# Kernel optimization log

Measured on AMD Instinct MI355X. Metric: run time of the kernel, lower is better.

## Reference

```python
import jax, jax.numpy as jnp
import numpy as np

N, E, DIN, DH, DOUT = 100000, 1600000, 512, 128, 40


def setup_inputs() -> dict:
    key = jax.random.key(0)
    ks = jax.random.split(key, 4)
    x = jax.random.normal(ks[0], (N, DIN), dtype=jnp.float32)
    edge_index = jax.random.randint(ks[1], (2, E), 0, N, dtype=jnp.int32)
    W1 = jax.random.normal(ks[2], (DIN, DH), dtype=jnp.float32) / np.sqrt(DIN).astype(np.float32)
    b1 = jnp.zeros((DH,), jnp.float32)
    W2 = jax.random.normal(ks[3], (DH, DOUT), dtype=jnp.float32) / np.sqrt(DH).astype(np.float32)
    b2 = jnp.zeros((DOUT,), jnp.float32)
    return {"x": x, "edge_index": edge_index, "W1": W1, "b1": b1, "W2": W2, "b2": b2}


def _gcn_conv(x, W, b, src, dst, norm, n):
    # PyG GCNConv: linear transform first, then normalized neighbor aggregation
    h = x @ W                                   # [n, d_out]
    msg = h[src] * norm[:, None]                # gather + scale, [E+n, d_out]
    out = jax.ops.segment_sum(msg, dst, num_segments=n)  # scatter-add
    return out + b


def reference(x, edge_index, W1, b1, W2, b2):
    n = x.shape[0]
    loops = jnp.arange(n, dtype=edge_index.dtype)
    src = jnp.concatenate([edge_index[0], loops])   # with self-loops
    dst = jnp.concatenate([edge_index[1], loops])
    deg = jax.ops.segment_sum(jnp.ones_like(dst, dtype=jnp.float32), dst, num_segments=n)
    dinv = jnp.where(deg > 0, jax.lax.rsqrt(jnp.maximum(deg, 1.0)), 0.0)
    norm = dinv[src] * dinv[dst]                    # deg^{-1/2}[j] * deg^{-1/2}[i]
    h = jax.nn.relu(_gcn_conv(x, W1, b1, src, dst, norm, n))
    # dropout p=0.5 is a no-op in eval mode (training=False)
    h = _gcn_conv(h, W2, b2, src, dst, norm, n)
    return h, jax.nn.log_softmax(h, axis=1)
```

## Files before the change

### kernel.cpp

```cpp
#include <hip/hip_runtime.h>
#include <math.h>


typedef unsigned int uint;
typedef unsigned short ushort_t;
using short8  = __attribute__((ext_vector_type(8))) short;
using float4v = __attribute__((ext_vector_type(4))) float;

__device__ __forceinline__ ushort_t f2bf(float f) {
    uint u = __float_as_uint(f);
    u += 0x7FFFu + ((u >> 16) & 1u);
    return (ushort_t)(u >> 16);
}
__device__ __forceinline__ float2 unpack2(uint v) {
    return make_float2(__uint_as_float(v << 16), __uint_as_float(v & 0xFFFF0000u));
}
__device__ __forceinline__ uint pack2(float a, float b) {
    return (uint)f2bf(a) | ((uint)f2bf(b) << 16);
}
__device__ __forceinline__ void acc8(float* acc, uint4 v) {
    float2 a0 = unpack2(v.x), a1 = unpack2(v.y), a2 = unpack2(v.z), a3 = unpack2(v.w);
    acc[0] += a0.x; acc[1] += a0.y; acc[2] += a1.x; acc[3] += a1.y;
    acc[4] += a2.x; acc[5] += a2.y; acc[6] += a3.x; acc[7] += a3.y;
}


__global__ __launch_bounds__(256) void k_bhist_wprep(const int* __restrict__ dst,
                                                     int* __restrict__ bcnt, int e, int nb,
                                                     int nblkA,
                                                     const float* __restrict__ W1,
                                                     const float* __restrict__ W2,
                                                     ushort_t* __restrict__ W1t,
                                                     ushort_t* __restrict__ W2t) {
    if (blockIdx.x >= (uint)nblkA) {
        int idx = (blockIdx.x - nblkA) * 256 + threadIdx.x;
        if (idx < 65536) {
            int nn = idx >> 9, k = idx & 511;
            W1t[idx] = f2bf(W1[(size_t)k * 128 + nn]);
        } else {
            int j = idx - 65536;
            if (j < 6144) {
                int c = j >> 7, k = j & 127;
                W2t[j] = (c < 40) ? f2bf(W2[(size_t)k * 40 + c]) : (ushort_t)0;
            }
        }
        return;
    }
    __shared__ int h[800];
    for (int t = threadIdx.x; t < nb; t += 256) h[t] = 0;
    __syncthreads();
    int ibase = blockIdx.x * 2560 + threadIdx.x;
#pragma unroll
    for (int j = 0; j < 10; j++) {
        int i = ibase + j * 256;
        if (i < e) atomicAdd(&h[dst[i] >> 7], 1);
    }
    __syncthreads();
    for (int t = threadIdx.x; t < nb; t += 256) {
        int c = h[t];
        if (c) atomicAdd(&bcnt[t], c);
    }
}

__global__ __launch_bounds__(256) void k_bscan(const int* __restrict__ bcnt, int* __restrict__ bbase,
                                               int* __restrict__ bcur, int* __restrict__ row_ptr,
                                               int nb, int n, int e) {
    __shared__ int sd[256];
    int t = threadIdx.x;
    int base = t * 4;
    int v[4];
#pragma unroll
    for (int j = 0; j < 4; j++) v[j] = (base + j < nb) ? bcnt[base + j] : 0;
    int s0 = v[0], s1 = s0 + v[1], s2 = s1 + v[2], s3 = s2 + v[3];
    sd[t] = s3;
    __syncthreads();
    for (int d = 1; d < 256; d <<= 1) {
        int x = (t >= d) ? sd[t - d] : 0;
        __syncthreads();
        sd[t] += x;
        __syncthreads();
    }
    int excl = sd[t] - s3;
    int pre0 = excl, pre1 = excl + s0, pre2 = excl + s1, pre3 = excl + s2;
    if (base + 0 < nb) { bbase[base + 0] = pre0; bcur[base + 0] = pre0; }
    if (base + 1 < nb) { bbase[base + 1] = pre1; bcur[base + 1] = pre1; }
    if (base + 2 < nb) { bbase[base + 2] = pre2; bcur[base + 2] = pre2; }
    if (base + 3 < nb) { bbase[base + 3] = pre3; bcur[base + 3] = pre3; }
    if (t == 255) bbase[nb] = excl + s3;
    if (t == 0) row_ptr[n] = e;
}

__global__ __launch_bounds__(256) void k_part(const int* __restrict__ src, const int* __restrict__ dst,
                                              int* __restrict__ bcur, uint* __restrict__ pbuf,
                                              int e, int nb) {
    __shared__ int h[800];
    __shared__ int base_l[800];
    for (int t = threadIdx.x; t < nb; t += 256) h[t] = 0;
    __syncthreads();
    uint pk[10]; int bk[10]; int lp[10];
    int ibase = blockIdx.x * 2560 + threadIdx.x;
#pragma unroll
    for (int j = 0; j < 10; j++) {
        int i = ibase + j * 256;
        bk[j] = -1;
        if (i < e) {
            int s = src[i], d = dst[i];
            int b = d >> 7;
            bk[j] = b;
            pk[j] = ((uint)(d & 127) << 25) | (uint)s;
            lp[j] = atomicAdd(&h[b], 1);
        }
    }
    __syncthreads();
    for (int t = threadIdx.x; t < nb; t += 256) {
        int c = h[t];
        base_l[t] = c ? atomicAdd(&bcur[t], c) : 0;
    }
    __syncthreads();
#pragma unroll
    for (int j = 0; j < 10; j++) {
        if (bk[j] >= 0) pbuf[base_l[bk[j]] + lp[j]] = pk[j];
    }
}

__global__ __launch_bounds__(256) void k_bsort(const uint* __restrict__ pbuf,
                                               const int* __restrict__ bbase,
                                               float* __restrict__ dinv,
                                               int* __restrict__ row_ptr,
                                               int* __restrict__ es_src, int n) {
    __shared__ int cl[128];
    __shared__ int cur[128];
    const int b = blockIdx.x;
    const int tid = threadIdx.x;
    const int ebeg = bbase[b], eend = bbase[b + 1];
    const int m = eend - ebeg;
    if (tid < 128) cl[tid] = 0;
    __syncthreads();
    for (int i = tid; i < m; i += 256) {
        uint p = pbuf[ebeg + i];
        atomicAdd(&cl[p >> 25], 1);
    }
    __syncthreads();
    int own = (tid < 128) ? cl[tid] : 0;
    for (int d = 1; d < 128; d <<= 1) {
        int v = 0;
        if (tid < 128 && tid >= d) v = cl[tid - d];
        __syncthreads();
        if (tid < 128 && tid >= d) cl[tid] += v;
        __syncthreads();
    }
    if (tid < 128) {
        int excl = cl[tid] - own;
        int node = b * 128 + tid;
        if (node < n) {
            dinv[node] = rsqrtf((float)(own + 1));
            row_ptr[node] = ebeg + excl;
        }
        cur[tid] = excl;
    }
    __syncthreads();
    for (int i = tid; i < m; i += 256) {
        uint p = pbuf[ebeg + i];
        int dl = (int)(p >> 25);
        int pos = atomicAdd(&cur[dl], 1);
        es_src[ebeg + pos] = (int)(p & 0x1FFFFFFu);
    }
}

__global__ __launch_bounds__(256) void k_gemm1(const float* __restrict__ x,
                                               const ushort_t* __restrict__ W1t,
                                               const float* __restrict__ dinv,
                                               ushort_t* __restrict__ h, int n) {
    __shared__ ushort_t As[64][72];
    __shared__ ushort_t Bs[128][72];
    const int tid  = threadIdx.x;
    const int w    = tid >> 6, lane = tid & 63;
    const int quad = lane >> 4, l16 = lane & 15;
    const int row0 = blockIdx.x * 64;

    float4v acc[8];
#pragma unroll
    for (int i = 0; i < 8; i++) acc[i] = (float4v)0.f;

    const int ar  = tid >> 2;
    const int akq = (tid & 3) * 16;
    const int br  = tid >> 1;
    const int bkq = (tid & 1) * 32;
    const int agrow = row0 + ar;
    const float* xp0 = &x[(size_t)agrow * 512];
    const ushort_t* wp0 = &W1t[(size_t)br * 512];

    for (int kb = 0; kb < 512; kb += 64) {
#pragma unroll
        for (int j = 0; j < 4; j++) {
            float4 v = make_float4(0.f, 0.f, 0.f, 0.f);
            if (agrow < n) v = *(const float4*)(xp0 + kb + akq + j * 4);
            ushort4 b;
            b.x = f2bf(v.x); b.y = f2bf(v.y); b.z = f2bf(v.z); b.w = f2bf(v.w);
            *(ushort4*)&As[ar][akq + j * 4] = b;
        }
#pragma unroll
        for (int j = 0; j < 8; j++) {
            *(ushort4*)&Bs[br][bkq + j * 4] = *(const ushort4*)(wp0 + kb + bkq + j * 4);
        }
        __syncthreads();
#pragma unroll
        for (int ks = 0; ks < 64; ks += 32) {
            short8 a = *(const short8*)&As[w * 16 + l16][ks + quad * 8];
#pragma unroll
            for (int ct = 0; ct < 8; ct++) {
                short8 b = *(const short8*)&Bs[ct * 16 + l16][ks + quad * 8];
                acc[ct] = __builtin_amdgcn_mfma_f32_16x16x32_bf16(a, b, acc[ct], 0, 0, 0);
            }
        }
        __syncthreads();
    }
#pragma unroll
    for (int r = 0; r < 4; r++) {
        int grow = row0 + w * 16 + quad * 4 + r;
        if (grow >= n) continue;
        float di = dinv[grow];
#pragma unroll
        for (int ct = 0; ct < 8; ct++) {
            int col = ct * 16 + l16;
            h[(size_t)grow * 128 + col] = f2bf(di * acc[ct][r]);
        }
    }
}

__global__ __launch_bounds__(256) void k_agg1(const uint* __restrict__ h,
                                              const int* __restrict__ row_ptr,
                                              const int* __restrict__ es_src,
                                              const float* __restrict__ dinv,
                                              const float* __restrict__ b1,
                                              uint* __restrict__ h1, int n) {
    const int tid  = threadIdx.x;
    const int node = blockIdx.x * 4 + (tid >> 6);
    if (node >= n) return;
    const int lane = tid & 63;
    const int g4   = lane >> 4;
    const int l16  = lane & 15;
    const int k0 = row_ptr[node], k1 = row_ptr[node + 1];

    uint4 sv = *(const uint4*)&h[(size_t)node * 64 + l16 * 4];

    float acc[8];
#pragma unroll
    for (int i = 0; i < 8; i++) acc[i] = 0.f;

    int k = k0 + g4;
    for (; k + 4 < k1; k += 8) {
        int s0 = es_src[k];
        int s1 = es_src[k + 4];
        uint4 v0 = *(const uint4*)&h[(size_t)s0 * 64 + l16 * 4];
        uint4 v1 = *(const uint4*)&h[(size_t)s1 * 64 + l16 * 4];
        acc8(acc, v0);
        acc8(acc, v1);
    }
    for (; k < k1; k += 4) {
        int s0 = es_src[k];
        uint4 v0 = *(const uint4*)&h[(size_t)s0 * 64 + l16 * 4];
        acc8(acc, v0);
    }

#pragma unroll
    for (int i = 0; i < 8; i++) {
        acc[i] += __shfl_xor(acc[i], 16);
        acc[i] += __shfl_xor(acc[i], 32);
    }
    acc8(acc, sv);

    const float di = dinv[node];
    float4 ba = *(const float4*)&b1[l16 * 8];
    float4 bb = *(const float4*)&b1[l16 * 8 + 4];
    float r[8];
    r[0] = di * acc[0] + ba.x; r[1] = di * acc[1] + ba.y;
    r[2] = di * acc[2] + ba.z; r[3] = di * acc[3] + ba.w;
    r[4] = di * acc[4] + bb.x; r[5] = di * acc[5] + bb.y;
    r[6] = di * acc[6] + bb.z; r[7] = di * acc[7] + bb.w;
#pragma unroll
    for (int i = 0; i < 8; i++) r[i] = r[i] > 0.f ? r[i] : 0.f;

    if (g4 == 0) {
        uint4 o;
        o.x = pack2(r[0], r[1]); o.y = pack2(r[2], r[3]);
        o.z = pack2(r[4], r[5]); o.w = pack2(r[6], r[7]);
        *(uint4*)&h1[(size_t)node * 64 + l16 * 4] = o;
    }
}

__global__ __launch_bounds__(256) void k_gemm2(const ushort_t* __restrict__ h1,
                                               const ushort_t* __restrict__ W2t,
                                               const float* __restrict__ dinv,
                                               ushort_t* __restrict__ g, int n) {
    __shared__ ushort_t As[64][136];
    __shared__ ushort_t Bs[48][136];
    const int tid  = threadIdx.x;
    const int w    = tid >> 6, lane = tid & 63;
    const int quad = lane >> 4, l16 = lane & 15;
    const int row0 = blockIdx.x * 64;

    {
        int ar = tid >> 2;
        int ak = (tid & 3) * 32;
        int grow = row0 + ar;
#pragma unroll
        for (int j = 0; j < 4; j++) {
            uint4 v = make_uint4(0, 0, 0, 0);
            if (grow < n) v = *(const uint4*)&h1[(size_t)grow * 128 + ak + j * 8];
            *(uint4*)&As[ar][ak + j * 8] = v;
        }
    }
    for (int i = tid; i < 768; i += 256) {
        int row = i >> 4, q = i & 15;
        *(uint4*)&Bs[row][q * 8] = *(const uint4*)&W2t[(size_t)row * 128 + q * 8];
    }
    __syncthreads();

    float4v acc[3];
#pragma unroll
    for (int i = 0; i < 3; i++) acc[i] = (float4v)0.f;
#pragma unroll
    for (int ks = 0; ks < 128; ks += 32) {
        short8 a = *(const short8*)&As[w * 16 + l16][ks + quad * 8];
#pragma unroll
        for (int ct = 0; ct < 3; ct++) {
            short8 b = *(const short8*)&Bs[ct * 16 + l16][ks + quad * 8];
            acc[ct] = __builtin_amdgcn_mfma_f32_16x16x32_bf16(a, b, acc[ct], 0, 0, 0);
        }
    }
#pragma unroll
    for (int r = 0; r < 4; r++) {
        int grow = row0 + w * 16 + quad * 4 + r;
        if (grow >= n) continue;
        float di = dinv[grow];
#pragma unroll
        for (int ct = 0; ct < 3; ct++) {
            int col = ct * 16 + l16;
            g[(size_t)grow * 64 + col] = f2bf(di * acc[ct][r]);
        }
        g[(size_t)grow * 64 + 48 + l16] = (ushort_t)0;
    }
}

__global__ __launch_bounds__(256) void k_agg2(const uint* __restrict__ g,
                                              const int* __restrict__ row_ptr,
                                              const int* __restrict__ es_src,
                                              const float* __restrict__ dinv,
                                              const float* __restrict__ b2,
                                              float* __restrict__ out1,
                                              float* __restrict__ out2, int n) {
    const int tid  = threadIdx.x;
    const int node = blockIdx.x * 4 + (tid >> 6);
    if (node >= n) return;
    const int lane = tid & 63;
    const int g8   = lane >> 3;
    const int l8   = lane & 7;
    const int k0 = row_ptr[node], k1 = row_ptr[node + 1];

    uint4 sv = *(const uint4*)&g[(size_t)node * 32 + l8 * 4];

    float acc[8];
#pragma unroll
    for (int i = 0; i < 8; i++) acc[i] = 0.f;

    int k = k0 + g8;
    for (; k + 8 < k1; k += 16) {
        int s0 = es_src[k];
        int s1 = es_src[k + 8];
        uint4 v0 = *(const uint4*)&g[(size_t)s0 * 32 + l8 * 4];
        uint4 v1 = *(const uint4*)&g[(size_t)s1 * 32 + l8 * 4];
        acc8(acc, v0);
        acc8(acc, v1);
    }
    for (; k < k1; k += 8) {
        int s0 = es_src[k];
        uint4 v0 = *(const uint4*)&g[(size_t)s0 * 32 + l8 * 4];
        acc8(acc, v0);
    }

#pragma unroll
    for (int i = 0; i < 8; i++) {
        acc[i] += __shfl_xor(acc[i], 8);
        acc[i] += __shfl_xor(acc[i], 16);
        acc[i] += __shfl_xor(acc[i], 32);
    }
    acc8(acc, sv);

    const float di = dinv[node];
    float v[8];
    if (l8 < 5) {
        float4 ba = *(const float4*)&b2[l8 * 8];
        float4 bb = *(const float4*)&b2[l8 * 8 + 4];
        v[0] = di * acc[0] + ba.x; v[1] = di * acc[1] + ba.y;
        v[2] = di * acc[2] + ba.z; v[3] = di * acc[3] + ba.w;
        v[4] = di * acc[4] + bb.x; v[5] = di * acc[5] + bb.y;
        v[6] = di * acc[6] + bb.z; v[7] = di * acc[7] + bb.w;
    } else {
#pragma unroll
        for (int i = 0; i < 8; i++) v[i] = 0.f;
    }

    float m = -1e30f;
    if (l8 < 5) {
#pragma unroll
        for (int i = 0; i < 8; i++) m = fmaxf(m, v[i]);
    }
#pragma unroll
    for (int d = 1; d < 8; d <<= 1) m = fmaxf(m, __shfl_xor(m, d));
    float s = 0.f;
    if (l8 < 5) {
#pragma unroll
        for (int i = 0; i < 8; i++) s += expf(v[i] - m);
    }
#pragma unroll
    for (int d = 1; d < 8; d <<= 1) s += __shfl_xor(s, d);
    float ls = logf(s) + m;

    if (l8 < 5) {
        if (g8 == 0) {
            *(float4*)&out1[(size_t)node * 40 + l8 * 8]     = make_float4(v[0], v[1], v[2], v[3]);
            *(float4*)&out1[(size_t)node * 40 + l8 * 8 + 4] = make_float4(v[4], v[5], v[6], v[7]);
        } else if (g8 == 1) {
            *(float4*)&out2[(size_t)node * 40 + l8 * 8] =
                make_float4(v[0] - ls, v[1] - ls, v[2] - ls, v[3] - ls);
            *(float4*)&out2[(size_t)node * 40 + l8 * 8 + 4] =
                make_float4(v[4] - ls, v[5] - ls, v[6] - ls, v[7] - ls);
        }
    }
}

static inline size_t align4(size_t v) { return (v + 3) & ~(size_t)3; }

extern "C" void kernel_launch(void* const* d_in, const int* in_sizes, int n_in,
                              void* d_out, int out_size, void* d_ws, size_t ws_size,
                              hipStream_t stream) {
    const float* x  = (const float*)d_in[0];
    const int*   ei = (const int*)d_in[1];
    const float* W1 = (const float*)d_in[2];
    const float* b1 = (const float*)d_in[3];
    const float* W2 = (const float*)d_in[4];
    const float* b2 = (const float*)d_in[5];

    const int n = in_sizes[0] / 512;
    const int e = in_sizes[1] / 2;
    const int* src = ei;
    const int* dst = ei + e;
    const int NB = (n + 127) >> 7;

    char* p = (char*)d_ws;
    int*      bcnt    = (int*)p;        p += align4(NB) * 4;
    int*      bbase   = (int*)p;        p += align4(NB + 1) * 4;
    int*      bcur    = (int*)p;        p += align4(NB) * 4;
    int*      row_ptr = (int*)p;        p += align4(n + 1) * 4;
    float*    dinv    = (float*)p;      p += align4(n) * 4;
    uint*     pbuf    = (uint*)p;       p += align4(e) * 4;
    int*      es_src  = (int*)p;        p += align4(e) * 4;
    ushort_t* W1t     = (ushort_t*)p;   p += (size_t)128 * 512 * 2;
    ushort_t* W2t     = (ushort_t*)p;   p += (size_t)48 * 128 * 2;
    ushort_t* h       = (ushort_t*)p;   p += (size_t)n * 128 * 2;
    ushort_t* h1      = (ushort_t*)p;   p += (size_t)n * 128 * 2;
    ushort_t* g       = h;
    float*    out1    = (float*)d_out;
    float*    out2    = out1 + (size_t)n * 40;

    const int B = 256;
    const int nblkA = (e + 2559) / 2560;

    hipMemsetAsync(bcnt, 0, (size_t)NB * 4, stream);
    k_bhist_wprep<<<nblkA + 280, B, 0, stream>>>(dst, bcnt, e, NB, nblkA, W1, W2, W1t, W2t);
    k_bscan<<<1, 256, 0, stream>>>(bcnt, bbase, bcur, row_ptr, NB, n, e);
    k_part<<<nblkA, B, 0, stream>>>(src, dst, bcur, pbuf, e, NB);
    k_bsort<<<NB, 256, 0, stream>>>(pbuf, bbase, dinv, row_ptr, es_src, n);

    k_gemm1<<<(n + 63) / 64, 256, 0, stream>>>(x, W1t, dinv, h, n);
    k_agg1<<<(n + 3) / 4, 256, 0, stream>>>((const uint*)h, row_ptr, es_src, dinv, b1, (uint*)h1, n);

    k_gemm2<<<(n + 63) / 64, 256, 0, stream>>>(h1, W2t, dinv, g, n);
    k_agg2<<<(n + 3) / 4, 256, 0, stream>>>((const uint*)g, row_ptr, es_src, dinv, b2, out1, out2, n);
}
```

Before: 535.1 us.

## Overlap GEMM1 with CSR build by splitting it across preprocessing kernels

Splits the first-layer GEMM into four chunks and appends each chunk as extra blocks to the histogram, scan, partition and bucket-sort kernels, so the compute-heavy GEMM runs alongside the latency-bound CSR construction. This removes GEMM1's dependency on dinv: the source-side dinv scaling moves into agg1 as a per-edge dinv gather with an FMA. The memset is folded into the weight-prep kernel. The cost is an extra random 4-byte dinv load per edge in agg1, plus larger shared-memory footprint and register pressure in the fused kernels, which may lower their occupancy.

```diff
diff --git a/kernel.cpp b/kernel.cpp
--- a/kernel.cpp
+++ b/kernel.cpp
@@ -23,48 +23,127 @@
     acc[0] += a0.x; acc[1] += a0.y; acc[2] += a1.x; acc[3] += a1.y;
     acc[4] += a2.x; acc[5] += a2.y; acc[6] += a3.x; acc[7] += a3.y;
 }
-
-
-__global__ __launch_bounds__(256) void k_bhist_wprep(const int* __restrict__ dst,
-                                                     int* __restrict__ bcnt, int e, int nb,
-                                                     int nblkA,
-                                                     const float* __restrict__ W1,
-                                                     const float* __restrict__ W2,
-                                                     ushort_t* __restrict__ W1t,
-                                                     ushort_t* __restrict__ W2t) {
-    if (blockIdx.x >= (uint)nblkA) {
-        int idx = (blockIdx.x - nblkA) * 256 + threadIdx.x;
-        if (idx < 65536) {
-            int nn = idx >> 9, k = idx & 511;
-            W1t[idx] = f2bf(W1[(size_t)k * 128 + nn]);
-        } else {
-            int j = idx - 65536;
-            if (j < 6144) {
-                int c = j >> 7, k = j & 127;
-                W2t[j] = (c < 40) ? f2bf(W2[(size_t)k * 40 + c]) : (ushort_t)0;
+__device__ __forceinline__ void acc8s(float* acc, uint4 v, float d) {
+    float2 a0 = unpack2(v.x), a1 = unpack2(v.y), a2 = unpack2(v.z), a3 = unpack2(v.w);
+    acc[0] = fmaf(d, a0.x, acc[0]); acc[1] = fmaf(d, a0.y, acc[1]);
+    acc[2] = fmaf(d, a1.x, acc[2]); acc[3] = fmaf(d, a1.y, acc[3]);
+    acc[4] = fmaf(d, a2.x, acc[4]); acc[5] = fmaf(d, a2.y, acc[5]);
+    acc[6] = fmaf(d, a3.x, acc[6]); acc[7] = fmaf(d, a3.y, acc[7]);
+}
+
+__device__ __forceinline__ void gemm1_block(int gb, const float* __restrict__ x,
+                                            const ushort_t* __restrict__ W1t,
+                                            ushort_t* __restrict__ h, int n) {
+    __shared__ ushort_t As[64][72];
+    __shared__ ushort_t Bs[128][72];
+    const int tid  = threadIdx.x;
+    const int w    = tid >> 6, lane = tid & 63;
+    const int quad = lane >> 4, l16 = lane & 15;
+    const int row0 = gb * 64;
+
+    float4v acc[8];
+#pragma unroll
+    for (int i = 0; i < 8; i++) acc[i] = (float4v)0.f;
+
+    const int ar  = tid >> 2;
+    const int akq = (tid & 3) * 16;
+    const int br  = tid >> 1;
+    const int bkq = (tid & 1) * 32;
+    const int agrow = row0 + ar;
+    const float* xp0 = &x[(size_t)agrow * 512];
+    const ushort_t* wp0 = &W1t[(size_t)br * 512];
+
+    for (int kb = 0; kb < 512; kb += 64) {
+#pragma unroll
+        for (int j = 0; j < 4; j++) {
+            float4 v = make_float4(0.f, 0.f, 0.f, 0.f);
+            if (agrow < n) v = *(const float4*)(xp0 + kb + akq + j * 4);
+            ushort4 b;
+            b.x = f2bf(v.x); b.y = f2bf(v.y); b.z = f2bf(v.z); b.w = f2bf(v.w);
+            *(ushort4*)&As[ar][akq + j * 4] = b;
+        }
+#pragma unroll
+        for (int j = 0; j < 8; j++) {
+            *(ushort4*)&Bs[br][bkq + j * 4] = *(const ushort4*)(wp0 + kb + bkq + j * 4);
+        }
+        __syncthreads();
+#pragma unroll
+        for (int ks = 0; ks < 64; ks += 32) {
+            short8 a = *(const short8*)&As[w * 16 + l16][ks + quad * 8];
+#pragma unroll
+            for (int ct = 0; ct < 8; ct++) {
+                short8 b = *(const short8*)&Bs[ct * 16 + l16][ks + quad * 8];
+                acc[ct] = __builtin_amdgcn_mfma_f32_16x16x32_bf16(a, b, acc[ct], 0, 0, 0);
             }
         }
+        __syncthreads();
+    }
+#pragma unroll
+    for (int r = 0; r < 4; r++) {
+        int grow = row0 + w * 16 + quad * 4 + r;
+        if (grow >= n) continue;
+#pragma unroll
+        for (int ct = 0; ct < 8; ct++) {
+            int col = ct * 16 + l16;
+            h[(size_t)grow * 128 + col] = f2bf(acc[ct][r]);
+        }
+    }
+}
+
+__global__ __launch_bounds__(256) void k_prep(const float* __restrict__ W1,
+                                              const float* __restrict__ W2,
+                                              ushort_t* __restrict__ W1t,
+                                              ushort_t* __restrict__ W2t,
+                                              int* __restrict__ bcnt, int nb) {
+    int idx = blockIdx.x * 256 + threadIdx.x;
+    if (idx < 65536) {
+        int nn = idx >> 9, k = idx & 511;
+        W1t[idx] = f2bf(W1[(size_t)k * 128 + nn]);
+    } else if (idx < 71680) {
+        int j = idx - 65536;
+        int c = j >> 7, k = j & 127;
+        W2t[j] = (c < 40) ? f2bf(W2[(size_t)k * 40 + c]) : (ushort_t)0;
+    } else {
+        int j = idx - 71680;
+        if (j < nb) bcnt[j] = 0;
+    }
+}
+
+__global__ __launch_bounds__(256) void k_d2(const int* __restrict__ dst,
+                                            int* __restrict__ bcnt, int e, int nb, int nblkA,
+                                            const float* __restrict__ x,
+                                            const ushort_t* __restrict__ W1t,
+                                            ushort_t* __restrict__ h, int n, int goff) {
+    if ((int)blockIdx.x >= nblkA) {
+        gemm1_block((int)blockIdx.x - nblkA + goff, x, W1t, h, n);
         return;
     }
-    __shared__ int h[800];
-    for (int t = threadIdx.x; t < nb; t += 256) h[t] = 0;
+    __shared__ int sh[800];
+    for (int t = threadIdx.x; t < nb; t += 256) sh[t] = 0;
     __syncthreads();
     int ibase = blockIdx.x * 2560 + threadIdx.x;
 #pragma unroll
     for (int j = 0; j < 10; j++) {
         int i = ibase + j * 256;
-        if (i < e) atomicAdd(&h[dst[i] >> 7], 1);
+        if (i < e) atomicAdd(&sh[dst[i] >> 7], 1);
     }
     __syncthreads();
     for (int t = threadIdx.x; t < nb; t += 256) {
-        int c = h[t];
+        int c = sh[t];
         if (c) atomicAdd(&bcnt[t], c);
     }
 }
 
-__global__ __launch_bounds__(256) void k_bscan(const int* __restrict__ bcnt, int* __restrict__ bbase,
-                                               int* __restrict__ bcur, int* __restrict__ row_ptr,
-                                               int nb, int n, int e) {
+__global__ __launch_bounds__(256) void k_d3(const int* __restrict__ bcnt, int* __restrict__ bbase,
+                                            int* __restrict__ bcur, int* __restrict__ row_ptr,
+                                            int nb, int n, int e,
+                                            const float* __restrict__ x,
+                                            const ushort_t* __restrict__ W1t,
+                                            ushort_t* __restrict__ h, int goff) {
+    if (blockIdx.x > 0) {
+        gemm1_block((int)blockIdx.x - 1 + goff, x, W1t, h, n);
+        return;
+    }
     __shared__ int sd[256];
     int t = threadIdx.x;
     int base = t * 4;
@@ -75,9 +154,9 @@
     sd[t] = s3;
     __syncthreads();
     for (int d = 1; d < 256; d <<= 1) {
-        int x = (t >= d) ? sd[t - d] : 0;
+        int xv = (t >= d) ? sd[t - d] : 0;
         __syncthreads();
-        sd[t] += x;
+        sd[t] += xv;
         __syncthreads();
     }
     int excl = sd[t] - s3;
@@ -90,12 +169,19 @@
     if (t == 0) row_ptr[n] = e;
 }
 
-__global__ __launch_bounds__(256) void k_part(const int* __restrict__ src, const int* __restrict__ dst,
-                                              int* __restrict__ bcur, uint* __restrict__ pbuf,
-                                              int e, int nb) {
-    __shared__ int h[800];
+__global__ __launch_bounds__(256) void k_d4(const int* __restrict__ src, const int* __restrict__ dst,
+                                            int* __restrict__ bcur, uint* __restrict__ pbuf,
+                                            int e, int nb, int nblkA,
+                                            const float* __restrict__ x,
+                                            const ushort_t* __restrict__ W1t,
+                                            ushort_t* __restrict__ h, int n, int goff) {
+    if ((int)blockIdx.x >= nblkA) {
+        gemm1_block((int)blockIdx.x - nblkA + goff, x, W1t, h, n);
+        return;
+    }
+    __shared__ int sh[800];
     __shared__ int base_l[800];
-    for (int t = threadIdx.x; t < nb; t += 256) h[t] = 0;
+    for (int t = threadIdx.x; t < nb; t += 256) sh[t] = 0;
     __syncthreads();
     uint pk[10]; int bk[10]; int lp[10];
     int ibase = blockIdx.x * 2560 + threadIdx.x;
@@ -108,12 +194,12 @@
             int b = d >> 7;
             bk[j] = b;
             pk[j] = ((uint)(d & 127) << 25) | (uint)s;
-            lp[j] = atomicAdd(&h[b], 1);
+            lp[j] = atomicAdd(&sh[b], 1);
         }
     }
     __syncthreads();
     for (int t = threadIdx.x; t < nb; t += 256) {
-        int c = h[t];
+        int c = sh[t];
         base_l[t] = c ? atomicAdd(&bcur[t], c) : 0;
     }
     __syncthreads();
@@ -123,11 +209,18 @@
     }
 }
 
-__global__ __launch_bounds__(256) void k_bsort(const uint* __restrict__ pbuf,
-                                               const int* __restrict__ bbase,
-                                               float* __restrict__ dinv,
-                                               int* __restrict__ row_ptr,
-                                               int* __restrict__ es_src, int n) {
+__global__ __launch_bounds__(256) void k_d5(const uint* __restrict__ pbuf,
+                                            const int* __restrict__ bbase,
+                                            float* __restrict__ dinv,
+                                            int* __restrict__ row_ptr,
+                                            int* __restrict__ es_src, int n, int nb,
+                                            const float* __restrict__ x,
+                                            const ushort_t* __restrict__ W1t,
+                                            ushort_t* __restrict__ h, int goff) {
+    if ((int)blockIdx.x >= nb) {
+        gemm1_block((int)blockIdx.x - nb + goff, x, W1t, h, n);
+        return;
+    }
     __shared__ int cl[128];
     __shared__ int cur[128];
     const int b = blockIdx.x;
@@ -164,67 +257,6 @@
         int dl = (int)(p >> 25);
         int pos = atomicAdd(&cur[dl], 1);
         es_src[ebeg + pos] = (int)(p & 0x1FFFFFFu);
-    }
-}
-
-__global__ __launch_bounds__(256) void k_gemm1(const float* __restrict__ x,
-                                               const ushort_t* __restrict__ W1t,
-                                               const float* __restrict__ dinv,
-                                               ushort_t* __restrict__ h, int n) {
-    __shared__ ushort_t As[64][72];
-    __shared__ ushort_t Bs[128][72];
-    const int tid  = threadIdx.x;
-    const int w    = tid >> 6, lane = tid & 63;
-    const int quad = lane >> 4, l16 = lane & 15;
-    const int row0 = blockIdx.x * 64;
-
-    float4v acc[8];
-#pragma unroll
-    for (int i = 0; i < 8; i++) acc[i] = (float4v)0.f;
-
-    const int ar  = tid >> 2;
-    const int akq = (tid & 3) * 16;
-    const int br  = tid >> 1;
-    const int bkq = (tid & 1) * 32;
-    const int agrow = row0 + ar;
-    const float* xp0 = &x[(size_t)agrow * 512];
-    const ushort_t* wp0 = &W1t[(size_t)br * 512];
-
-    for (int kb = 0; kb < 512; kb += 64) {
-#pragma unroll
-        for (int j = 0; j < 4; j++) {
-            float4 v = make_float4(0.f, 0.f, 0.f, 0.f);
-            if (agrow < n) v = *(const float4*)(xp0 + kb + akq + j * 4);
-            ushort4 b;
-            b.x = f2bf(v.x); b.y = f2bf(v.y); b.z = f2bf(v.z); b.w = f2bf(v.w);
-            *(ushort4*)&As[ar][akq + j * 4] = b;
-        }
-#pragma unroll
-        for (int j = 0; j < 8; j++) {
-            *(ushort4*)&Bs[br][bkq + j * 4] = *(const ushort4*)(wp0 + kb + bkq + j * 4);
-        }
-        __syncthreads();
-#pragma unroll
-        for (int ks = 0; ks < 64; ks += 32) {
-            short8 a = *(const short8*)&As[w * 16 + l16][ks + quad * 8];
-#pragma unroll
-            for (int ct = 0; ct < 8; ct++) {
-                short8 b = *(const short8*)&Bs[ct * 16 + l16][ks + quad * 8];
-                acc[ct] = __builtin_amdgcn_mfma_f32_16x16x32_bf16(a, b, acc[ct], 0, 0, 0);
-            }
-        }
-        __syncthreads();
-    }
-#pragma unroll
-    for (int r = 0; r < 4; r++) {
-        int grow = row0 + w * 16 + quad * 4 + r;
-        if (grow >= n) continue;
-        float di = dinv[grow];
-#pragma unroll
-        for (int ct = 0; ct < 8; ct++) {
-            int col = ct * 16 + l16;
-            h[(size_t)grow * 128 + col] = f2bf(di * acc[ct][r]);
-        }
     }
 }
 
@@ -241,6 +273,7 @@
     const int g4   = lane >> 4;
     const int l16  = lane & 15;
     const int k0 = row_ptr[node], k1 = row_ptr[node + 1];
+    const float di = dinv[node];
 
     uint4 sv = *(const uint4*)&h[(size_t)node * 64 + l16 * 4];
 
@@ -252,15 +285,17 @@
     for (; k + 4 < k1; k += 8) {
         int s0 = es_src[k];
         int s1 = es_src[k + 4];
+        float d0 = dinv[s0], d1 = dinv[s1];
         uint4 v0 = *(const uint4*)&h[(size_t)s0 * 64 + l16 * 4];
         uint4 v1 = *(const uint4*)&h[(size_t)s1 * 64 + l16 * 4];
-        acc8(acc, v0);
-        acc8(acc, v1);
+        acc8s(acc, v0, d0);
+        acc8s(acc, v1, d1);
     }
     for (; k < k1; k += 4) {
         int s0 = es_src[k];
+        float d0 = dinv[s0];
         uint4 v0 = *(const uint4*)&h[(size_t)s0 * 64 + l16 * 4];
-        acc8(acc, v0);
+        acc8s(acc, v0, d0);
     }
 
 #pragma unroll
@@ -268,9 +303,8 @@
         acc[i] += __shfl_xor(acc[i], 16);
         acc[i] += __shfl_xor(acc[i], 32);
     }
-    acc8(acc, sv);
-
-    const float di = dinv[node];
+    acc8s(acc, sv, di);
+
     float4 ba = *(const float4*)&b1[l16 * 8];
     float4 bb = *(const float4*)&b1[l16 * 8 + 4];
     float r[8];
@@ -466,16 +500,19 @@
 
     const int B = 256;
     const int nblkA = (e + 2559) / 2560;
-
-    hipMemsetAsync(bcnt, 0, (size_t)NB * 4, stream);
-    k_bhist_wprep<<<nblkA + 280, B, 0, stream>>>(dst, bcnt, e, NB, nblkA, W1, W2, W1t, W2t);
-    k_bscan<<<1, 256, 0, stream>>>(bcnt, bbase, bcur, row_ptr, NB, n, e);
-    k_part<<<nblkA, B, 0, stream>>>(src, dst, bcur, pbuf, e, NB);
-    k_bsort<<<NB, 256, 0, stream>>>(pbuf, bbase, dinv, row_ptr, es_src, n);
-
-    k_gemm1<<<(n + 63) / 64, 256, 0, stream>>>(x, W1t, dinv, h, n);
-    k_agg1<<<(n + 3) / 4, 256, 0, stream>>>((const uint*)h, row_ptr, es_src, dinv, b1, (uint*)h1, n);
-
-    k_gemm2<<<(n + 63) / 64, 256, 0, stream>>>(h1, W2t, dinv, g, n);
-    k_agg2<<<(n + 3) / 4, 256, 0, stream>>>((const uint*)g, row_ptr, es_src, dinv, b2, out1, out2, n);
-}
+    const int NG = (n + 63) / 64;
+    const int c  = (NG + 3) / 4;
+    const int c3 = NG - 3 * c;
+
+    k_prep<<<(71680 + NB + 255) / 256, B, 0, stream>>>(W1, W2, W1t, W2t, bcnt, NB);
+
+    k_d2<<<nblkA + c, B, 0, stream>>>(dst, bcnt, e, NB, nblkA, x, W1t, h, n, 0);
+    k_d3<<<1 + c, B, 0, stream>>>(bcnt, bbase, bcur, row_ptr, NB, n, e, x, W1t, h, c);
+    k_d4<<<nblkA + c, B, 0, stream>>>(src, dst, bcur, pbuf, e, NB, nblkA, x, W1t, h, n, 2 * c);
+    k_d5<<<NB + c3, B, 0, stream>>>(pbuf, bbase, dinv, row_ptr, es_src, n, NB, x, W1t, h, 3 * c);
+
+    k_agg1<<<(n + 3) / 4, B, 0, stream>>>((const uint*)h, row_ptr, es_src, dinv, b1, (uint*)h1, n);
+
+    k_gemm2<<<(n + 63) / 64, B, 0, stream>>>(h1, W2t, dinv, g, n);
+    k_agg2<<<(n + 3) / 4, B, 0, stream>>>((const uint*)g, row_ptr, es_src, dinv, b2, out1, out2, n);
+}
```

Result: faster. 518.4 us (-3.1%).
